# Optimization experiments

Hardware: AMD Instinct MI355X
Metric: run time of the kernel (lower is better)

The kernel has to match this reference:

```python
import jax, jax.numpy as jnp
import numpy as np

B, T, C, H = 256, 256, 384, 64  # batch, seq (== block_size), n_embd, head_size


def setup_inputs() -> dict:
    key = jax.random.key(0)
    kx, kk, kq, kv = jax.random.split(key, 4)
    scale = C ** -0.5
    x = jax.random.normal(kx, (B, T, C), dtype=jnp.float32)
    Wk = jax.random.normal(kk, (C, H), dtype=jnp.float32) * scale
    Wq = jax.random.normal(kq, (C, H), dtype=jnp.float32) * scale
    Wv = jax.random.normal(kv, (C, H), dtype=jnp.float32) * scale
    return {"x": x, "Wk": Wk, "Wq": Wq, "Wv": Wv}


def reference(x, Wk, Wq, Wv):
    # Single causal self-attention head (x_kv=None path). Dropout is eval-mode (identity).
    Tn = x.shape[1]
    k = x @ Wk            # [B, T, H]
    q = x @ Wq            # [B, T, H]
    v = x @ Wv            # [B, T, H]
    inv_sqrt_d = k.shape[-1] ** -0.5
    wei = jnp.einsum('bth,bsh->bts', q, k) * inv_sqrt_d  # [B, T, T]
    causal = jnp.tril(jnp.ones((Tn, Tn), dtype=bool))
    wei = jnp.where(causal, wei, -jnp.inf)
    wei = jax.nn.softmax(wei, axis=-1)
    out = jnp.einsum('bts,bsh->bth', wei, v)             # [B, T, H]
    return out
```

## Files before the change

### kernel.cpp

```cpp
#include <hip/hip_runtime.h>

#define BATCH 256
#define SEQ   256
#define CDIM  384
#define HDIM  64

typedef __attribute__((ext_vector_type(8))) short bf16x8;
typedef __attribute__((ext_vector_type(4))) float f32x4;

__device__ __forceinline__ unsigned f2bf(float f) {
  union { float f; unsigned u; } v; v.f = f;
  unsigned r = v.u + 0x7FFFu + ((v.u >> 16) & 1u);
  return r >> 16;
}

__global__ void wtrans_kernel(const float* __restrict__ Wk, const float* __restrict__ Wq,
                              const float* __restrict__ Wv, unsigned short* __restrict__ WTf) {
  int gid = blockIdx.x * 256 + threadIdx.x;
  if (gid >= 192 * CDIM) return;
  int n = gid / CDIM, kk = gid - n * CDIM;
  const float* W = (n < 64) ? Wq : (n < 128) ? Wk : Wv;
  int nt = n >> 4, ln = n & 15, ks = kk >> 5, sub = (kk >> 3) & 3, j = kk & 7;
  int lane = ln + 16 * sub;
  WTf[(((size_t)ks * 12 + nt) * 64 + lane) * 8 + j] =
      (unsigned short)f2bf(W[kk * HDIM + (n & 63)]);
}

__global__ __launch_bounds__(512, 2) void fused_kernel(
    const float* __restrict__ x, const unsigned short* __restrict__ WTf,
    float* __restrict__ out) {
  __shared__ unsigned short lds[73728];
  const int tid = threadIdx.x, b = blockIdx.x;
  const int w = tid >> 6, lane = tid & 63;
  const int ln15 = lane & 15, quad = lane >> 4;

  {
    const uint4* src = (const uint4*)WTf;
    uint4* dst = (uint4*)lds;
    #pragma unroll
    for (int i = 0; i < 18; ++i) dst[i * 512 + tid] = src[i * 512 + tid];
  }

  bf16x8 bx[2][12];
  {
    const float* xr0 = x + (size_t)(b * 256 + w * 32 + ln15) * CDIM + quad * 8;
    #pragma unroll
    for (int rg = 0; rg < 2; ++rg) {
      const float* xr = xr0 + rg * 16 * CDIM;
      #pragma unroll
      for (int hh = 0; hh < 2; ++hh) {
        float4 A[12];
        #pragma unroll
        for (int j = 0; j < 6; ++j) {
          A[2 * j]     = *(const float4*)(xr + (hh * 6 + j) * 32);
          A[2 * j + 1] = *(const float4*)(xr + (hh * 6 + j) * 32 + 4);
        }
        #pragma unroll
        for (int j = 0; j < 6; ++j) {
          bf16x8 t;
          t[0] = (short)f2bf(A[2 * j].x);     t[1] = (short)f2bf(A[2 * j].y);
          t[2] = (short)f2bf(A[2 * j].z);     t[3] = (short)f2bf(A[2 * j].w);
          t[4] = (short)f2bf(A[2 * j + 1].x); t[5] = (short)f2bf(A[2 * j + 1].y);
          t[6] = (short)f2bf(A[2 * j + 1].z); t[7] = (short)f2bf(A[2 * j + 1].w);
          bx[rg][hh * 6 + j] = t;
        }
      }
    }
  }

  __syncthreads();

  f32x4 acc[2][12];
  #pragma unroll
  for (int rg = 0; rg < 2; ++rg)
    #pragma unroll
    for (int nt = 0; nt < 12; ++nt) acc[rg][nt] = (f32x4){0.f, 0.f, 0.f, 0.f};

  #pragma unroll
  for (int ks = 0; ks < 12; ++ks) {
    #pragma unroll
    for (int nt = 0; nt < 12; ++nt) {
      bf16x8 aw = *(const bf16x8*)&lds[((ks * 12 + nt) * 64 + lane) * 8];
      acc[0][nt] = __builtin_amdgcn_mfma_f32_16x16x32_bf16(aw, bx[0][ks], acc[0][nt], 0, 0, 0);
      acc[1][nt] = __builtin_amdgcn_mfma_f32_16x16x32_bf16(aw, bx[1][ks], acc[1][nt], 0, 0, 0);
    }
  }

  __syncthreads();

  unsigned short (*QL)[72]  = (unsigned short(*)[72])lds;
  unsigned short (*KL)[72]  = (unsigned short(*)[72])(lds + 18432);
  unsigned short (*VT)[264] = (unsigned short(*)[264])(lds + 36864);
  unsigned short (*PL)[36]  = (unsigned short(*)[36])(lds + 53760 + w * 576);

  #pragma unroll
  for (int rg = 0; rg < 2; ++rg) {
    const int trow = w * 32 + rg * 16 + ln15;
    #pragma unroll
    for (int nt = 0; nt < 4; ++nt) {
      f32x4 a = acc[rg][nt];
      unsigned p0 = f2bf(a[0]) | (f2bf(a[1]) << 16);
      unsigned p1 = f2bf(a[2]) | (f2bf(a[3]) << 16);
      *(uint2*)&QL[trow][nt * 16 + quad * 4] = (uint2){p0, p1};
    }
    #pragma unroll
    for (int nt = 4; nt < 8; ++nt) {
      f32x4 a = acc[rg][nt];
      unsigned p0 = f2bf(a[0]) | (f2bf(a[1]) << 16);
      unsigned p1 = f2bf(a[2]) | (f2bf(a[3]) << 16);
      *(uint2*)&KL[trow][(nt - 4) * 16 + quad * 4] = (uint2){p0, p1};
    }
    #pragma unroll
    for (int nt = 8; nt < 12; ++nt) {
      f32x4 a = acc[rg][nt];
      const int h = (nt - 8) * 16 + quad * 4;
      #pragma unroll
      for (int i = 0; i < 4; ++i)
        VT[h + i][trow] = (unsigned short)f2bf(a[i]);
    }
  }
  __syncthreads();

  for (int mi = 0; mi < 2; ++mi) {
    const int mt = mi ? (15 - w) : w;
    const int t0 = mt * 16;
    const int NT = (mt | 1) + 1;

    bf16x8 aq[2];
    #pragma unroll
    for (int ks = 0; ks < 2; ++ks)
      aq[ks] = *(const bf16x8*)&QL[t0 + ln15][ks * 32 + quad * 8];

    float sv[16][4];
    #pragma unroll
    for (int nt = 0; nt < 16; ++nt) {
      if (nt < NT) {
        f32x4 a2 = (f32x4){0.f, 0.f, 0.f, 0.f};
        #pragma unroll
        for (int ks = 0; ks < 2; ++ks) {
          bf16x8 bf = *(const bf16x8*)&KL[nt * 16 + ln15][ks * 32 + quad * 8];
          a2 = __builtin_amdgcn_mfma_f32_16x16x32_bf16(aq[ks], bf, a2, 0, 0, 0);
        }
        int colg = nt * 16 + ln15;
        #pragma unroll
        for (int i = 0; i < 4; ++i) {
          int rowg = t0 + quad * 4 + i;
          sv[nt][i] = (colg <= rowg) ? a2[i] * 0.125f : -3.0e38f;
        }
      }
    }
    float mx[4] = {-3.0e38f, -3.0e38f, -3.0e38f, -3.0e38f};
    #pragma unroll
    for (int nt = 0; nt < 16; ++nt)
      if (nt < NT) {
        #pragma unroll
        for (int i = 0; i < 4; ++i) mx[i] = fmaxf(mx[i], sv[nt][i]);
      }
    #pragma unroll
    for (int i = 0; i < 4; ++i) {
      mx[i] = fmaxf(mx[i], __shfl_xor(mx[i], 8, 64));
      mx[i] = fmaxf(mx[i], __shfl_xor(mx[i], 4, 64));
      mx[i] = fmaxf(mx[i], __shfl_xor(mx[i], 2, 64));
      mx[i] = fmaxf(mx[i], __shfl_xor(mx[i], 1, 64));
    }
    float sm[4] = {0.f, 0.f, 0.f, 0.f};
    #pragma unroll
    for (int nt = 0; nt < 16; ++nt)
      if (nt < NT) {
        #pragma unroll
        for (int i = 0; i < 4; ++i) {
          float e = __expf(sv[nt][i] - mx[i]);
          sv[nt][i] = e;
          sm[i] += e;
        }
      }
    #pragma unroll
    for (int i = 0; i < 4; ++i) {
      sm[i] += __shfl_xor(sm[i], 8, 64);
      sm[i] += __shfl_xor(sm[i], 4, 64);
      sm[i] += __shfl_xor(sm[i], 2, 64);
      sm[i] += __shfl_xor(sm[i], 1, 64);
    }
    float inv[4];
    #pragma unroll
    for (int i = 0; i < 4; ++i) inv[i] = 1.0f / sm[i];

    f32x4 o[4];
    #pragma unroll
    for (int ont = 0; ont < 4; ++ont) o[ont] = (f32x4){0.f, 0.f, 0.f, 0.f};

    #pragma unroll
    for (int kc = 0; kc < 8; ++kc) {
      if (kc * 2 < NT) {
        #pragma unroll
        for (int half = 0; half < 2; ++half) {
          int nt = kc * 2 + half;
          #pragma unroll
          for (int i = 0; i < 4; ++i)
            PL[quad * 4 + i][half * 16 + ln15] =
                (unsigned short)f2bf(sv[nt][i] * inv[i]);
        }
        bf16x8 pa = *(const bf16x8*)&PL[ln15][quad * 8];
        #pragma unroll
        for (int ont = 0; ont < 4; ++ont) {
          bf16x8 vb = *(const bf16x8*)&VT[ont * 16 + ln15][kc * 32 + quad * 8];
          o[ont] = __builtin_amdgcn_mfma_f32_16x16x32_bf16(pa, vb, o[ont], 0, 0, 0);
        }
      }
    }

    #pragma unroll
    for (int ont = 0; ont < 4; ++ont) {
      int h = ont * 16 + ln15;
      #pragma unroll
      for (int i = 0; i < 4; ++i)
        out[(size_t)(b * 256 + t0 + quad * 4 + i) * HDIM + h] = o[ont][i];
    }
  }
}

extern "C" void kernel_launch(void* const* d_in, const int* in_sizes, int n_in,
                              void* d_out, int out_size, void* d_ws, size_t ws_size,
                              hipStream_t stream) {
  const float* x  = (const float*)d_in[0];
  const float* Wk = (const float*)d_in[1];
  const float* Wq = (const float*)d_in[2];
  const float* Wv = (const float*)d_in[3];
  float* out = (float*)d_out;

  unsigned short* WTf = (unsigned short*)d_ws;

  wtrans_kernel<<<(192 * CDIM + 255) / 256, 256, 0, stream>>>(Wk, Wq, Wv, WTf);
  fused_kernel<<<256, 512, 0, stream>>>(x, WTf, out);
}
```

Baseline: 190.0 us.

## Double block size to one row tile per wave and load weights directly to LDS

Launches 1024-thread blocks so each of 16 waves computes the QKV projection for 16 rows and handles one causal query tile. This replaces the previous two-tiles-per-wave scheme that paired tile w with tile 15-w. The weight copy into LDS now uses global_load_lds, skipping the trip through registers. The aim is more waves per CU to hide latency, but causal work is no longer balanced across waves. The launch bound of 1024 threads with 4 blocks per multiprocessor may force a tight register budget and cause spills.

```diff
diff --git a/kernel.cpp b/kernel.cpp
--- a/kernel.cpp
+++ b/kernel.cpp
@@ -26,63 +26,61 @@
       (unsigned short)f2bf(W[kk * HDIM + (n & 63)]);
 }
 
-__global__ __launch_bounds__(512, 2) void fused_kernel(
+__global__ __launch_bounds__(1024, 4) void fused_kernel(
     const float* __restrict__ x, const unsigned short* __restrict__ WTf,
     float* __restrict__ out) {
-  __shared__ unsigned short lds[73728];
+  __shared__ __align__(16) unsigned short lds[73728];
   const int tid = threadIdx.x, b = blockIdx.x;
   const int w = tid >> 6, lane = tid & 63;
   const int ln15 = lane & 15, quad = lane >> 4;
 
   {
     const uint4* src = (const uint4*)WTf;
-    uint4* dst = (uint4*)lds;
-    #pragma unroll
-    for (int i = 0; i < 18; ++i) dst[i * 512 + tid] = src[i * 512 + tid];
-  }
-
-  bf16x8 bx[2][12];
-  {
-    const float* xr0 = x + (size_t)(b * 256 + w * 32 + ln15) * CDIM + quad * 8;
-    #pragma unroll
-    for (int rg = 0; rg < 2; ++rg) {
-      const float* xr = xr0 + rg * 16 * CDIM;
-      #pragma unroll
-      for (int hh = 0; hh < 2; ++hh) {
-        float4 A[12];
-        #pragma unroll
-        for (int j = 0; j < 6; ++j) {
-          A[2 * j]     = *(const float4*)(xr + (hh * 6 + j) * 32);
-          A[2 * j + 1] = *(const float4*)(xr + (hh * 6 + j) * 32 + 4);
-        }
-        #pragma unroll
-        for (int j = 0; j < 6; ++j) {
-          bf16x8 t;
-          t[0] = (short)f2bf(A[2 * j].x);     t[1] = (short)f2bf(A[2 * j].y);
-          t[2] = (short)f2bf(A[2 * j].z);     t[3] = (short)f2bf(A[2 * j].w);
-          t[4] = (short)f2bf(A[2 * j + 1].x); t[5] = (short)f2bf(A[2 * j + 1].y);
-          t[6] = (short)f2bf(A[2 * j + 1].z); t[7] = (short)f2bf(A[2 * j + 1].w);
-          bx[rg][hh * 6 + j] = t;
-        }
+    #pragma unroll
+    for (int i = 0; i < 9; ++i) {
+      int c = i * 1024 + tid;
+      __builtin_amdgcn_global_load_lds(
+          (const __attribute__((address_space(1))) unsigned*)(src + c),
+          (__attribute__((address_space(3))) unsigned*)((char*)lds + (size_t)c * 16),
+          16, 0, 0);
+    }
+  }
+
+  bf16x8 bx[12];
+  {
+    const float* xr = x + (size_t)(b * 256 + w * 16 + ln15) * CDIM + quad * 8;
+    #pragma unroll
+    for (int hh = 0; hh < 2; ++hh) {
+      float4 A[12];
+      #pragma unroll
+      for (int j = 0; j < 6; ++j) {
+        A[2 * j]     = *(const float4*)(xr + (hh * 6 + j) * 32);
+        A[2 * j + 1] = *(const float4*)(xr + (hh * 6 + j) * 32 + 4);
+      }
+      #pragma unroll
+      for (int j = 0; j < 6; ++j) {
+        bf16x8 t;
+        t[0] = (short)f2bf(A[2 * j].x);     t[1] = (short)f2bf(A[2 * j].y);
+        t[2] = (short)f2bf(A[2 * j].z);     t[3] = (short)f2bf(A[2 * j].w);
+        t[4] = (short)f2bf(A[2 * j + 1].x); t[5] = (short)f2bf(A[2 * j + 1].y);
+        t[6] = (short)f2bf(A[2 * j + 1].z); t[7] = (short)f2bf(A[2 * j + 1].w);
+        bx[hh * 6 + j] = t;
       }
     }
   }
 
   __syncthreads();
 
-  f32x4 acc[2][12];
+  f32x4 acc[12];
   #pragma unroll
-  for (int rg = 0; rg < 2; ++rg)
-    #pragma unroll
-    for (int nt = 0; nt < 12; ++nt) acc[rg][nt] = (f32x4){0.f, 0.f, 0.f, 0.f};
+  for (int nt = 0; nt < 12; ++nt) acc[nt] = (f32x4){0.f, 0.f, 0.f, 0.f};
 
   #pragma unroll
   for (int ks = 0; ks < 12; ++ks) {
     #pragma unroll
     for (int nt = 0; nt < 12; ++nt) {
       bf16x8 aw = *(const bf16x8*)&lds[((ks * 12 + nt) * 64 + lane) * 8];
-      acc[0][nt] = __builtin_amdgcn_mfma_f32_16x16x32_bf16(aw, bx[0][ks], acc[0][nt], 0, 0, 0);
-      acc[1][nt] = __builtin_amdgcn_mfma_f32_16x16x32_bf16(aw, bx[1][ks], acc[1][nt], 0, 0, 0);
+      acc[nt] = __builtin_amdgcn_mfma_f32_16x16x32_bf16(aw, bx[ks], acc[nt], 0, 0, 0);
     }
   }
 
@@ -93,26 +91,25 @@
   unsigned short (*VT)[264] = (unsigned short(*)[264])(lds + 36864);
   unsigned short (*PL)[36]  = (unsigned short(*)[36])(lds + 53760 + w * 576);
 
-  #pragma unroll
-  for (int rg = 0; rg < 2; ++rg) {
-    const int trow = w * 32 + rg * 16 + ln15;
+  {
+    const int trow = w * 16 + ln15;
     #pragma unroll
     for (int nt = 0; nt < 4; ++nt) {
-      f32x4 a = acc[rg][nt];
+      f32x4 a = acc[nt];
       unsigned p0 = f2bf(a[0]) | (f2bf(a[1]) << 16);
       unsigned p1 = f2bf(a[2]) | (f2bf(a[3]) << 16);
       *(uint2*)&QL[trow][nt * 16 + quad * 4] = (uint2){p0, p1};
     }
     #pragma unroll
     for (int nt = 4; nt < 8; ++nt) {
-      f32x4 a = acc[rg][nt];
+      f32x4 a = acc[nt];
       unsigned p0 = f2bf(a[0]) | (f2bf(a[1]) << 16);
       unsigned p1 = f2bf(a[2]) | (f2bf(a[3]) << 16);
       *(uint2*)&KL[trow][(nt - 4) * 16 + quad * 4] = (uint2){p0, p1};
     }
     #pragma unroll
     for (int nt = 8; nt < 12; ++nt) {
-      f32x4 a = acc[rg][nt];
+      f32x4 a = acc[nt];
       const int h = (nt - 8) * 16 + quad * 4;
       #pragma unroll
       for (int i = 0; i < 4; ++i)
@@ -121,8 +118,8 @@
   }
   __syncthreads();
 
-  for (int mi = 0; mi < 2; ++mi) {
-    const int mt = mi ? (15 - w) : w;
+  {
+    const int mt = w;
     const int t0 = mt * 16;
     const int NT = (mt | 1) + 1;
 
@@ -231,5 +228,5 @@
   unsigned short* WTf = (unsigned short*)d_ws;
 
   wtrans_kernel<<<(192 * CDIM + 255) / 256, 256, 0, stream>>>(Wk, Wq, Wv, WTf);
-  fused_kernel<<<256, 512, 0, stream>>>(x, WTf, out);
-}
+  fused_kernel<<<256, 1024, 0, stream>>>(x, WTf, out);
+}
```

Measured after the change: 181.3 us. 4.6% less time.
